# Performance work log

Measured on AMD Instinct MI355X. Metric: run time of the kernel, lower is better.

The kernel has to match this reference:

```python
import jax, jax.numpy as jnp
import numpy as np

NMS_THRESH = 0.7
N_PRE = 12000
N_POST = 2000
IMG_X, IMG_Y = 1333.0, 402.0
MIN_SIZE = 16.0
FEAT_X, FEAT_Y, N_ANCH = 83, 25, 9   # int(1333/16), int(402/16), 9 anchors/cell
A = FEAT_X * FEAT_Y * N_ANCH         # 18675 anchors
CHUNK = 600                          # N_PRE % CHUNK == 0 -> 20 scan steps


def _make_anchors():
    stride = 16.0
    scales = np.array([8.0, 16.0, 32.0])
    ratios = np.array([0.5, 1.0, 2.0])
    hs = (stride * scales[:, None] * np.sqrt(ratios)[None, :]).ravel()  # 9 heights
    ws = (stride * scales[:, None] / np.sqrt(ratios)[None, :]).ravel()  # 9 widths
    cx = (np.arange(FEAT_X, dtype=np.float64) + 0.5) * stride
    cy = (np.arange(FEAT_Y, dtype=np.float64) + 0.5) * stride
    cxg, cyg = np.meshgrid(cx, cy, indexing="ij")  # [83,25]
    cxg = cxg[:, :, None]
    cyg = cyg[:, :, None]
    boxes = np.stack([cxg - 0.5 * ws, cyg - 0.5 * hs,
                      cxg + 0.5 * ws, cyg + 0.5 * hs], axis=-1)  # [83,25,9,4]
    return boxes.reshape(-1, 4).astype(np.float32)


def setup_inputs() -> dict:
    key = jax.random.key(0)
    k1, k2 = jax.random.split(key)
    return {
        "anchor_boxes": jnp.asarray(_make_anchors()),                          # [A,4]
        "rpn_cls_score": jax.random.normal(k1, (1, A, 2), jnp.float32),        # [B,A,2]
        "rpn_bbox_pred": jax.random.normal(k2, (1, A, 4), jnp.float32) * 0.1,  # [B,A,4]
    }


def _decode(anchor_boxes, rpn_cls_score, rpn_bbox_pred):
    # anchor geometry (same conventions as original: y from col1/3, x from col0/2)
    h_a = anchor_boxes[:, 3] - anchor_boxes[:, 1]
    w_a = anchor_boxes[:, 2] - anchor_boxes[:, 0]
    cy_a = anchor_boxes[:, 1] + 0.5 * h_a
    cx_a = anchor_boxes[:, 0] + 0.5 * w_a
    dx = rpn_bbox_pred[..., 0]
    dy = rpn_bbox_pred[..., 1]
    dw = rpn_bbox_pred[..., 2]
    dh = rpn_bbox_pred[..., 3]
    cy = dy * h_a + cy_a
    cx = dx * w_a + cx_a
    h = jnp.exp(dh) * h_a
    w = jnp.exp(dw) * w_a
    # clip: x coords to image_size[0], y coords to image_size[1] (as in original)
    x1 = jnp.clip(cx - 0.5 * w, 0.0, IMG_X)
    x2 = jnp.clip(cx + 0.5 * w, 0.0, IMG_X)
    y1 = jnp.clip(cy - 0.5 * h, 0.0, IMG_Y)
    y2 = jnp.clip(cy + 0.5 * h, 0.0, IMG_Y)
    roi = jnp.stack([x1, y1, x2, y2], axis=-1)  # [B,A,4]
    valid = ((y2 - y1) >= MIN_SIZE) & ((x2 - x1) >= MIN_SIZE)  # [B,A]
    score = rpn_cls_score[..., 1]  # objectness = channel 1 of 2-class score
    return roi, score, valid


def _nms_per_image(roi, score, valid):
    # sort valid boxes by descending score, take top N_PRE
    score = jnp.where(valid, score, -jnp.inf)
    order = jnp.argsort(-score)[:N_PRE]
    boxes = roi[order]  # [N_PRE,4]
    x1, y1, x2, y2 = boxes[:, 0], boxes[:, 1], boxes[:, 2], boxes[:, 3]
    areas = (x2 - x1 + 1.0) * (y2 - y1 + 1.0)
    idx = jnp.arange(N_PRE)

    def chunk_step(mark, zs):
        def row(z):
            xx1 = jnp.maximum(x1[z], x1)
            yy1 = jnp.maximum(y1[z], y1)
            xx2 = jnp.minimum(x2[z], x2)
            yy2 = jnp.minimum(y2[z], y2)
            w = jnp.maximum(0.0, xx2 - xx1 + 1.0)
            h = jnp.maximum(0.0, yy2 - yy1 + 1.0)
            inter = w * h
            ovr = inter / (areas[z] + areas - inter)
            over = ovr >= NMS_THRESH
            # faithful to original: np.where on the slice [z+1:] yields indices
            # RELATIVE to the slice, which are then used as absolute row indices.
            # So box k is deleted iff exists z with IoU(box z, box z+1+k) >= thresh.
            src = idx + z + 1
            contrib = jnp.where(src < N_PRE, over[jnp.minimum(src, N_PRE - 1)], False)
            return contrib & (z < N_PRE - 1)  # loop runs z in range(N_PRE-1)
        contribs = jax.vmap(row)(zs)  # [CHUNK, N_PRE]
        return mark | contribs.any(axis=0), None

    mark0 = jnp.zeros((N_PRE,), bool)
    mark, _ = jax.lax.scan(chunk_step, mark0, idx.reshape(-1, CHUNK))
    keep = ~mark
    # compact kept boxes to the front (stable), truncate to N_POST
    ord2 = jnp.argsort((~keep).astype(jnp.int32), stable=True)[:N_POST]
    kept = keep[ord2]
    out = jnp.where(kept[:, None], boxes[ord2], 0.0)  # zero-pad deleted slots
    return out, kept


def reference(anchor_boxes, rpn_cls_score, rpn_bbox_pred):
    roi, score, valid = _decode(anchor_boxes, rpn_cls_score, rpn_bbox_pred)
    rois, kept = jax.vmap(_nms_per_image)(roi, score, valid)
    return rois, kept  # [B,N_POST,4], [B,N_POST]
```

## Files before the change

kernel.cpp:

```cpp
#include <hip/hip_runtime.h>
#include <math.h>

#define A_TOT   18675
#define N_PRE   12000
#define N_POST  2000
#define IMG_X   1333.0f
#define IMG_Y   402.0f
#define MIN_SZ  16.0f
#define NMS_T   0.7f
#define NBUCK   4096
#define NBLK1   19

__global__ __launch_bounds__(1024)
void decode_hist_kernel(const float* __restrict__ anch,
                        const float* __restrict__ cls,
                        const float* __restrict__ pred,
                        float4* __restrict__ roi,
                        unsigned long long* __restrict__ key,
                        unsigned* __restrict__ phist,
                        unsigned* __restrict__ gcnt) {
    __shared__ unsigned lh[NBUCK];
    const int t   = threadIdx.x;
    const int blk = blockIdx.x;
    const int g   = blk * 1024 + t;

#pragma unroll
    for (int e = 0; e < 4; ++e) lh[t + e * 1024] = 0u;
    if (g < NBUCK) gcnt[g] = 0u;
    __syncthreads();

    if (g < A_TOT) {
        float ax1 = anch[4*g+0], ay1 = anch[4*g+1], ax2 = anch[4*g+2], ay2 = anch[4*g+3];
        float h_a  = __fsub_rn(ay2, ay1);
        float w_a  = __fsub_rn(ax2, ax1);
        float cy_a = __fadd_rn(ay1, __fmul_rn(0.5f, h_a));
        float cx_a = __fadd_rn(ax1, __fmul_rn(0.5f, w_a));

        float dx = pred[4*g+0], dy = pred[4*g+1], dw = pred[4*g+2], dh = pred[4*g+3];

        float cy = __fadd_rn(__fmul_rn(dy, h_a), cy_a);
        float cx = __fadd_rn(__fmul_rn(dx, w_a), cx_a);
        float h  = __fmul_rn(expf(dh), h_a);
        float w  = __fmul_rn(expf(dw), w_a);

        float hw = __fmul_rn(0.5f, w);
        float hh = __fmul_rn(0.5f, h);
        float x1 = fminf(fmaxf(__fsub_rn(cx, hw), 0.0f), IMG_X);
        float x2 = fminf(fmaxf(__fadd_rn(cx, hw), 0.0f), IMG_X);
        float y1 = fminf(fmaxf(__fsub_rn(cy, hh), 0.0f), IMG_Y);
        float y2 = fminf(fmaxf(__fadd_rn(cy, hh), 0.0f), IMG_Y);

        bool valid = (__fsub_rn(y2, y1) >= MIN_SZ) && (__fsub_rn(x2, x1) >= MIN_SZ);

        roi[g] = make_float4(x1, y1, x2, y2);

        float s = valid ? cls[2*g+1] : -INFINITY;
        unsigned ub   = __float_as_uint(s);
        unsigned mask = ((unsigned)((int)ub >> 31)) | 0x80000000u;
        unsigned ord  = ub ^ mask;
        unsigned kd   = ~ord;
        key[g] = ((unsigned long long)kd << 32) | (unsigned)g;
        atomicAdd(&lh[kd >> 20], 1u);
    }
    __syncthreads();

    ((uint4*)phist)[blk * 1024 + t] =
        make_uint4(lh[4*t+0], lh[4*t+1], lh[4*t+2], lh[4*t+3]);
}

__global__ __launch_bounds__(1024)
void scan_scatter_kernel(const unsigned long long* __restrict__ key,
                         const unsigned* __restrict__ phist,
                         unsigned* __restrict__ gcnt,
                         unsigned* __restrict__ ghist,
                         unsigned* __restrict__ gbstart,
                         unsigned long long* __restrict__ bkey) {
    __shared__ unsigned bs[NBUCK];
    __shared__ unsigned wsum[16];
    const int t    = threadIdx.x;
    const int blk  = blockIdx.x;
    const int lane = t & 63;
    const int wv   = t >> 6;

    unsigned c0 = 0, c1 = 0, c2 = 0, c3 = 0;
#pragma unroll
    for (int k = 0; k < NBLK1; ++k) {
        uint4 v = ((const uint4*)phist)[k * 1024 + t];
        c0 += v.x; c1 += v.y; c2 += v.z; c3 += v.w;
    }
    unsigned mysum = c0 + c1 + c2 + c3;

    unsigned incl = mysum;
#pragma unroll
    for (int off = 1; off < 64; off <<= 1) {
        unsigned v = __shfl_up(incl, off, 64);
        if (lane >= off) incl += v;
    }
    if (lane == 63) wsum[wv] = incl;
    __syncthreads();
    if (t == 0) {
        unsigned run = 0;
        for (int k = 0; k < 16; ++k) { unsigned v = wsum[k]; wsum[k] = run; run += v; }
    }
    __syncthreads();

    unsigned base = wsum[wv] + (incl - mysum);
    unsigned s0 = base, s1 = s0 + c0, s2 = s1 + c1, s3 = s2 + c2;
    bs[4*t+0] = s0; bs[4*t+1] = s1; bs[4*t+2] = s2; bs[4*t+3] = s3;

    if (blk == 0) {
        ((uint4*)gbstart)[t] = make_uint4(s0, s1, s2, s3);
        ((uint4*)ghist)[t]   = make_uint4(c0, c1, c2, c3);
    }
    __syncthreads();

    int g = blk * 1024 + t;
    if (g < A_TOT) {
        unsigned long long Ki = key[g];
        unsigned b = (unsigned)(Ki >> 52);
        unsigned pos = bs[b] + atomicAdd(&gcnt[b], 1u);
        bkey[pos] = Ki;
    }
}

__global__ void rankscatter_kernel(const unsigned long long* __restrict__ bkey,
                                   const unsigned* __restrict__ gbstart,
                                   const unsigned* __restrict__ ghist,
                                   const float4* __restrict__ roi,
                                   float4* __restrict__ sboxes,
                                   float* __restrict__ sareas) {
    int g = blockIdx.x * blockDim.x + threadIdx.x;
    int p = g >> 6;
    int lane = g & 63;
    if (p >= A_TOT) return;

    unsigned long long Ki = bkey[p];
    unsigned b = (unsigned)(Ki >> 52);
    unsigned start = gbstart[b];
    if (start >= N_PRE) return;
    unsigned cnt = ghist[b];

    unsigned r = start;
    for (unsigned m = 0; m < cnt; m += 64) {
        unsigned mm = m + lane;
        bool lt = (mm < cnt) && (bkey[start + mm] < Ki);
        r += (unsigned)__popcll(__ballot(lt));
    }

    if (lane == 0 && r < N_PRE) {
        unsigned idx = (unsigned)Ki;
        float4 bx = roi[idx];
        sboxes[r] = bx;
        sareas[r] = __fmul_rn(__fadd_rn(__fsub_rn(bx.z, bx.x), 1.0f),
                              __fadd_rn(__fsub_rn(bx.w, bx.y), 1.0f));
    }
}

__global__ void nms_kernel(const float4* __restrict__ sboxes,
                           const float* __restrict__ sareas,
                           unsigned* __restrict__ mark) {
    int wid  = (blockIdx.x * blockDim.x + threadIdx.x) >> 6;
    int lane = threadIdx.x & 63;
    if (wid >= N_PRE) return;
    const int i      = wid;
    const int npairs = N_PRE - 1 - i;

    bool found = false;
    for (int base = 0; base < npairs; base += 64) {
        int z = base + lane;
        bool over = false;
        if (z < npairs) {
            float4 bz = sboxes[z];
            float4 bj = sboxes[z + i + 1];
            float az = sareas[z];
            float aj = sareas[z + i + 1];
            float xx1 = fmaxf(bz.x, bj.x);
            float yy1 = fmaxf(bz.y, bj.y);
            float xx2 = fminf(bz.z, bj.z);
            float yy2 = fminf(bz.w, bj.w);
            float w = fmaxf(0.0f, __fadd_rn(__fsub_rn(xx2, xx1), 1.0f));
            float h = fmaxf(0.0f, __fadd_rn(__fsub_rn(yy2, yy1), 1.0f));
            float inter = __fmul_rn(w, h);
            float denom = __fsub_rn(__fadd_rn(az, aj), inter);
            float ovr   = __fdiv_rn(inter, denom);
            over = (ovr >= NMS_T);
        }
        if (__any(over)) { found = true; break; }
    }
    if (lane == 0) mark[i] = found ? 1u : 0u;
}

__global__ __launch_bounds__(1024)
void output_kernel(const unsigned* __restrict__ mark,
                   const float4* __restrict__ sboxes,
                   float* __restrict__ out) {
    __shared__ int wsA[16];
    __shared__ int wsB[16];
    __shared__ int wsS[16];
    __shared__ int s_base, s_total;
    const int t    = threadIdx.x;
    const int blk  = blockIdx.x;
    const int lane = t & 63;
    const int wv   = t >> 6;
    const int limit = blk * 1024;

    int sum_before = 0, sum_total = 0;
    for (int j = t; j < N_PRE; j += 1024) {
        int k = (mark[j] == 0u) ? 1 : 0;
        sum_total += k;
        if (j < limit) sum_before += k;
    }
#pragma unroll
    for (int off = 32; off > 0; off >>= 1) {
        sum_before += __shfl_xor(sum_before, off, 64);
        sum_total  += __shfl_xor(sum_total,  off, 64);
    }
    if (lane == 0) { wsA[wv] = sum_before; wsB[wv] = sum_total; }
    __syncthreads();
    if (t == 0) {
        int a = 0, b = 0;
        for (int k = 0; k < 16; ++k) { a += wsA[k]; b += wsB[k]; }
        s_base = a; s_total = b;
    }
    __syncthreads();

    const int i = blk * 1024 + t;
    int keep = (i < N_PRE) && (mark[i] == 0u);

    int incl = keep;
#pragma unroll
    for (int off = 1; off < 64; off <<= 1) {
        int v = __shfl_up(incl, off, 64);
        if (lane >= off) incl += v;
    }
    if (lane == 63) wsS[wv] = incl;
    __syncthreads();
    if (t == 0) {
        int run = 0;
        for (int k = 0; k < 16; ++k) { int v = wsS[k]; wsS[k] = run; run += v; }
    }
    __syncthreads();

    int pos = s_base + wsS[wv] + (incl - keep);
    if (keep && pos < N_POST) {
        float4 b4 = sboxes[i];
        out[4*pos+0] = b4.x;
        out[4*pos+1] = b4.y;
        out[4*pos+2] = b4.z;
        out[4*pos+3] = b4.w;
        out[4*N_POST + pos] = 1.0f;
    }
    if (i < N_POST && i >= s_total) {
        out[4*i+0] = 0.0f; out[4*i+1] = 0.0f;
        out[4*i+2] = 0.0f; out[4*i+3] = 0.0f;
        out[4*N_POST + i] = 0.0f;
    }
}

extern "C" void kernel_launch(void* const* d_in, const int* in_sizes, int n_in,
                              void* d_out, int out_size, void* d_ws, size_t ws_size,
                              hipStream_t stream) {
    const float* anch = (const float*)d_in[0];
    const float* cls  = (const float*)d_in[1];
    const float* pred = (const float*)d_in[2];
    float* out = (float*)d_out;

    char* ws = (char*)d_ws;
    float4*             roi     = (float4*)(ws + 0);
    unsigned long long* key     = (unsigned long long*)(ws + 299008);
    unsigned*           phist   = (unsigned*)(ws + 448512);
    unsigned*           gcnt    = (unsigned*)(ws + 759808);
    unsigned*           ghist   = (unsigned*)(ws + 776192);
    unsigned*           gbstart = (unsigned*)(ws + 792576);
    unsigned long long* bkey    = (unsigned long long*)(ws + 808960);
    float4*             sboxes  = (float4*)(ws + 958464);
    float*              sareas  = (float*)(ws + 1150464);
    unsigned*           mark    = (unsigned*)(ws + 1198464);

    const int TB = 256;
    const int rblk = (A_TOT * 64 + TB - 1) / TB;

    decode_hist_kernel<<<NBLK1, 1024, 0, stream>>>(anch, cls, pred, roi, key, phist, gcnt);
    scan_scatter_kernel<<<NBLK1, 1024, 0, stream>>>(key, phist, gcnt, ghist, gbstart, bkey);
    rankscatter_kernel<<<rblk, TB, 0, stream>>>(bkey, gbstart, ghist, roi, sboxes, sareas);
    nms_kernel<<<(N_PRE * 64) / TB, TB, 0, stream>>>(sboxes, sareas, mark);
    output_kernel<<<12, 1024, 0, stream>>>(mark, sboxes, out);
}
```

Before: 57.96 us.

## Fuse all proposal stages into one cooperative kernel with grid-wide syncs

Replaces the five separate launches (decode/histogram, scan/scatter, rank-scatter, NMS, output compaction) with a single cooperative kernel of 256 blocks of 1024 threads that separates the stages with grid.sync(). The per-block partial histograms become one global histogram built with global atomics, and every block recomputes the bucket prefix scan in shared memory. The rank and NMS loops become grid-stride loops over waves. This removes four kernel launch gaps and the partial-histogram pass. In exchange it adds grid-wide barriers, contended global atomics and a cooperative launch whose 256x1024 residency must be supported.

After: 177.7 us. 207% more time.

```diff
diff --git a/kernel.cpp b/kernel.cpp
--- a/kernel.cpp
+++ b/kernel.cpp
@@ -1,4 +1,5 @@
 #include <hip/hip_runtime.h>
+#include <hip/hip_cooperative_groups.h>
 #include <math.h>
 
 #define A_TOT   18675
@@ -9,25 +10,43 @@
 #define MIN_SZ  16.0f
 #define NMS_T   0.7f
 #define NBUCK   4096
-#define NBLK1   19
-
-__global__ __launch_bounds__(1024)
-void decode_hist_kernel(const float* __restrict__ anch,
-                        const float* __restrict__ cls,
-                        const float* __restrict__ pred,
-                        float4* __restrict__ roi,
-                        unsigned long long* __restrict__ key,
-                        unsigned* __restrict__ phist,
-                        unsigned* __restrict__ gcnt) {
-    __shared__ unsigned lh[NBUCK];
-    const int t   = threadIdx.x;
-    const int blk = blockIdx.x;
-    const int g   = blk * 1024 + t;
-
-#pragma unroll
-    for (int e = 0; e < 4; ++e) lh[t + e * 1024] = 0u;
-    if (g < NBUCK) gcnt[g] = 0u;
-    __syncthreads();
+#define GBLK    256
+#define NTHR    1024
+#define NWAVES  (GBLK * (NTHR / 64))
+
+namespace cg = cooperative_groups;
+
+__global__ __launch_bounds__(NTHR)
+void fused_kernel(const float* __restrict__ anch,
+                  const float* __restrict__ cls,
+                  const float* __restrict__ pred,
+                  float4* __restrict__ roi,
+                  unsigned long long* __restrict__ key,
+                  unsigned* __restrict__ ghist,
+                  unsigned* __restrict__ gcnt,
+                  unsigned long long* __restrict__ bkey,
+                  float4* __restrict__ sboxes,
+                  float* __restrict__ sareas,
+                  unsigned* __restrict__ mark,
+                  float* __restrict__ out)
+{
+    cg::grid_group grid = cg::this_grid();
+
+    __shared__ unsigned bs[NBUCK];
+    __shared__ unsigned lcnt[NBUCK];
+    __shared__ unsigned wsum[16];
+    __shared__ int wsA[16], wsB[16], wsS[16];
+    __shared__ int s_base, s_total;
+
+    const int t    = threadIdx.x;
+    const int blk  = blockIdx.x;
+    const int g    = blk * NTHR + t;
+    const int lane = t & 63;
+    const int wv   = t >> 6;
+    const int gw   = blk * (NTHR / 64) + wv;
+
+    if (g < NBUCK) { ghist[g] = 0u; gcnt[g] = 0u; }
+    grid.sync();
 
     if (g < A_TOT) {
         float ax1 = anch[4*g+0], ay1 = anch[4*g+1], ax2 = anch[4*g+2], ay2 = anch[4*g+3];
@@ -60,200 +79,148 @@
         unsigned ord  = ub ^ mask;
         unsigned kd   = ~ord;
         key[g] = ((unsigned long long)kd << 32) | (unsigned)g;
-        atomicAdd(&lh[kd >> 20], 1u);
-    }
-    __syncthreads();
-
-    ((uint4*)phist)[blk * 1024 + t] =
-        make_uint4(lh[4*t+0], lh[4*t+1], lh[4*t+2], lh[4*t+3]);
-}
-
-__global__ __launch_bounds__(1024)
-void scan_scatter_kernel(const unsigned long long* __restrict__ key,
-                         const unsigned* __restrict__ phist,
-                         unsigned* __restrict__ gcnt,
-                         unsigned* __restrict__ ghist,
-                         unsigned* __restrict__ gbstart,
-                         unsigned long long* __restrict__ bkey) {
-    __shared__ unsigned bs[NBUCK];
-    __shared__ unsigned wsum[16];
-    const int t    = threadIdx.x;
-    const int blk  = blockIdx.x;
-    const int lane = t & 63;
-    const int wv   = t >> 6;
-
-    unsigned c0 = 0, c1 = 0, c2 = 0, c3 = 0;
+        atomicAdd(&ghist[kd >> 20], 1u);
+    }
+    grid.sync();
+
+    {
+        uint4 v = ((const uint4*)ghist)[t];
+        unsigned c0 = v.x, c1 = v.y, c2 = v.z, c3 = v.w;
+        unsigned mysum = c0 + c1 + c2 + c3;
+        unsigned incl = mysum;
 #pragma unroll
-    for (int k = 0; k < NBLK1; ++k) {
-        uint4 v = ((const uint4*)phist)[k * 1024 + t];
-        c0 += v.x; c1 += v.y; c2 += v.z; c3 += v.w;
-    }
-    unsigned mysum = c0 + c1 + c2 + c3;
-
-    unsigned incl = mysum;
-#pragma unroll
-    for (int off = 1; off < 64; off <<= 1) {
-        unsigned v = __shfl_up(incl, off, 64);
-        if (lane >= off) incl += v;
-    }
-    if (lane == 63) wsum[wv] = incl;
-    __syncthreads();
-    if (t == 0) {
-        unsigned run = 0;
-        for (int k = 0; k < 16; ++k) { unsigned v = wsum[k]; wsum[k] = run; run += v; }
-    }
-    __syncthreads();
-
-    unsigned base = wsum[wv] + (incl - mysum);
-    unsigned s0 = base, s1 = s0 + c0, s2 = s1 + c1, s3 = s2 + c2;
-    bs[4*t+0] = s0; bs[4*t+1] = s1; bs[4*t+2] = s2; bs[4*t+3] = s3;
-
-    if (blk == 0) {
-        ((uint4*)gbstart)[t] = make_uint4(s0, s1, s2, s3);
-        ((uint4*)ghist)[t]   = make_uint4(c0, c1, c2, c3);
-    }
-    __syncthreads();
-
-    int g = blk * 1024 + t;
+        for (int off = 1; off < 64; off <<= 1) {
+            unsigned x = __shfl_up(incl, off, 64);
+            if (lane >= off) incl += x;
+        }
+        if (lane == 63) wsum[wv] = incl;
+        __syncthreads();
+        if (t == 0) {
+            unsigned run = 0;
+            for (int k = 0; k < 16; ++k) { unsigned x = wsum[k]; wsum[k] = run; run += x; }
+        }
+        __syncthreads();
+        unsigned base = wsum[wv] + (incl - mysum);
+        bs[4*t+0] = base;
+        bs[4*t+1] = base + c0;
+        bs[4*t+2] = base + c0 + c1;
+        bs[4*t+3] = base + c0 + c1 + c2;
+        lcnt[4*t+0] = c0; lcnt[4*t+1] = c1; lcnt[4*t+2] = c2; lcnt[4*t+3] = c3;
+        __syncthreads();
+    }
+
     if (g < A_TOT) {
         unsigned long long Ki = key[g];
         unsigned b = (unsigned)(Ki >> 52);
         unsigned pos = bs[b] + atomicAdd(&gcnt[b], 1u);
         bkey[pos] = Ki;
     }
-}
-
-__global__ void rankscatter_kernel(const unsigned long long* __restrict__ bkey,
-                                   const unsigned* __restrict__ gbstart,
-                                   const unsigned* __restrict__ ghist,
-                                   const float4* __restrict__ roi,
-                                   float4* __restrict__ sboxes,
-                                   float* __restrict__ sareas) {
-    int g = blockIdx.x * blockDim.x + threadIdx.x;
-    int p = g >> 6;
-    int lane = g & 63;
-    if (p >= A_TOT) return;
-
-    unsigned long long Ki = bkey[p];
-    unsigned b = (unsigned)(Ki >> 52);
-    unsigned start = gbstart[b];
-    if (start >= N_PRE) return;
-    unsigned cnt = ghist[b];
-
-    unsigned r = start;
-    for (unsigned m = 0; m < cnt; m += 64) {
-        unsigned mm = m + lane;
-        bool lt = (mm < cnt) && (bkey[start + mm] < Ki);
-        r += (unsigned)__popcll(__ballot(lt));
-    }
-
-    if (lane == 0 && r < N_PRE) {
-        unsigned idx = (unsigned)Ki;
-        float4 bx = roi[idx];
-        sboxes[r] = bx;
-        sareas[r] = __fmul_rn(__fadd_rn(__fsub_rn(bx.z, bx.x), 1.0f),
-                              __fadd_rn(__fsub_rn(bx.w, bx.y), 1.0f));
-    }
-}
-
-__global__ void nms_kernel(const float4* __restrict__ sboxes,
-                           const float* __restrict__ sareas,
-                           unsigned* __restrict__ mark) {
-    int wid  = (blockIdx.x * blockDim.x + threadIdx.x) >> 6;
-    int lane = threadIdx.x & 63;
-    if (wid >= N_PRE) return;
-    const int i      = wid;
-    const int npairs = N_PRE - 1 - i;
-
-    bool found = false;
-    for (int base = 0; base < npairs; base += 64) {
-        int z = base + lane;
-        bool over = false;
-        if (z < npairs) {
-            float4 bz = sboxes[z];
-            float4 bj = sboxes[z + i + 1];
-            float az = sareas[z];
-            float aj = sareas[z + i + 1];
-            float xx1 = fmaxf(bz.x, bj.x);
-            float yy1 = fmaxf(bz.y, bj.y);
-            float xx2 = fminf(bz.z, bj.z);
-            float yy2 = fminf(bz.w, bj.w);
-            float w = fmaxf(0.0f, __fadd_rn(__fsub_rn(xx2, xx1), 1.0f));
-            float h = fmaxf(0.0f, __fadd_rn(__fsub_rn(yy2, yy1), 1.0f));
-            float inter = __fmul_rn(w, h);
-            float denom = __fsub_rn(__fadd_rn(az, aj), inter);
-            float ovr   = __fdiv_rn(inter, denom);
-            over = (ovr >= NMS_T);
-        }
-        if (__any(over)) { found = true; break; }
-    }
-    if (lane == 0) mark[i] = found ? 1u : 0u;
-}
-
-__global__ __launch_bounds__(1024)
-void output_kernel(const unsigned* __restrict__ mark,
-                   const float4* __restrict__ sboxes,
-                   float* __restrict__ out) {
-    __shared__ int wsA[16];
-    __shared__ int wsB[16];
-    __shared__ int wsS[16];
-    __shared__ int s_base, s_total;
-    const int t    = threadIdx.x;
-    const int blk  = blockIdx.x;
-    const int lane = t & 63;
-    const int wv   = t >> 6;
-    const int limit = blk * 1024;
-
-    int sum_before = 0, sum_total = 0;
-    for (int j = t; j < N_PRE; j += 1024) {
-        int k = (mark[j] == 0u) ? 1 : 0;
-        sum_total += k;
-        if (j < limit) sum_before += k;
-    }
+    grid.sync();
+
+    for (int p = gw; p < A_TOT; p += NWAVES) {
+        unsigned long long Ki = bkey[p];
+        unsigned b = (unsigned)(Ki >> 52);
+        unsigned start = bs[b];
+        if (start >= N_PRE) continue;
+        unsigned cnt = lcnt[b];
+        unsigned r = start;
+        for (unsigned m = 0; m < cnt; m += 64) {
+            unsigned mm = m + lane;
+            bool lt = (mm < cnt) && (bkey[start + mm] < Ki);
+            r += (unsigned)__popcll(__ballot(lt));
+        }
+        if (lane == 0 && r < N_PRE) {
+            unsigned idx = (unsigned)Ki;
+            float4 bx = roi[idx];
+            sboxes[r] = bx;
+            sareas[r] = __fmul_rn(__fadd_rn(__fsub_rn(bx.z, bx.x), 1.0f),
+                                  __fadd_rn(__fsub_rn(bx.w, bx.y), 1.0f));
+        }
+    }
+    grid.sync();
+
+    for (int i = gw; i < N_PRE; i += NWAVES) {
+        const int npairs = N_PRE - 1 - i;
+        bool found = false;
+        for (int base0 = 0; base0 < npairs; base0 += 64) {
+            int z = base0 + lane;
+            bool over = false;
+            if (z < npairs) {
+                float4 bz = sboxes[z];
+                float4 bj = sboxes[z + i + 1];
+                float az = sareas[z];
+                float aj = sareas[z + i + 1];
+                float xx1 = fmaxf(bz.x, bj.x);
+                float yy1 = fmaxf(bz.y, bj.y);
+                float xx2 = fminf(bz.z, bj.z);
+                float yy2 = fminf(bz.w, bj.w);
+                float w = fmaxf(0.0f, __fadd_rn(__fsub_rn(xx2, xx1), 1.0f));
+                float h = fmaxf(0.0f, __fadd_rn(__fsub_rn(yy2, yy1), 1.0f));
+                float inter = __fmul_rn(w, h);
+                float denom = __fsub_rn(__fadd_rn(az, aj), inter);
+                float ovr   = __fdiv_rn(inter, denom);
+                over = (ovr >= NMS_T);
+            }
+            if (__any(over)) { found = true; break; }
+        }
+        if (lane == 0) mark[i] = found ? 1u : 0u;
+    }
+    grid.sync();
+
+    if (blk < 12) {
+        const int limit = blk * NTHR;
+
+        int sum_before = 0, sum_total = 0;
+        for (int j = t; j < N_PRE; j += NTHR) {
+            int k = (mark[j] == 0u) ? 1 : 0;
+            sum_total += k;
+            if (j < limit) sum_before += k;
+        }
 #pragma unroll
-    for (int off = 32; off > 0; off >>= 1) {
-        sum_before += __shfl_xor(sum_before, off, 64);
-        sum_total  += __shfl_xor(sum_total,  off, 64);
-    }
-    if (lane == 0) { wsA[wv] = sum_before; wsB[wv] = sum_total; }
-    __syncthreads();
-    if (t == 0) {
-        int a = 0, b = 0;
-        for (int k = 0; k < 16; ++k) { a += wsA[k]; b += wsB[k]; }
-        s_base = a; s_total = b;
-    }
-    __syncthreads();
-
-    const int i = blk * 1024 + t;
-    int keep = (i < N_PRE) && (mark[i] == 0u);
-
-    int incl = keep;
+        for (int off = 32; off > 0; off >>= 1) {
+            sum_before += __shfl_xor(sum_before, off, 64);
+            sum_total  += __shfl_xor(sum_total,  off, 64);
+        }
+        if (lane == 0) { wsA[wv] = sum_before; wsB[wv] = sum_total; }
+        __syncthreads();
+        if (t == 0) {
+            int a = 0, b = 0;
+            for (int k = 0; k < 16; ++k) { a += wsA[k]; b += wsB[k]; }
+            s_base = a; s_total = b;
+        }
+        __syncthreads();
+
+        const int i = blk * NTHR + t;
+        int keep = (i < N_PRE) && (mark[i] == 0u);
+
+        int incl = keep;
 #pragma unroll
-    for (int off = 1; off < 64; off <<= 1) {
-        int v = __shfl_up(incl, off, 64);
-        if (lane >= off) incl += v;
-    }
-    if (lane == 63) wsS[wv] = incl;
-    __syncthreads();
-    if (t == 0) {
-        int run = 0;
-        for (int k = 0; k < 16; ++k) { int v = wsS[k]; wsS[k] = run; run += v; }
-    }
-    __syncthreads();
-
-    int pos = s_base + wsS[wv] + (incl - keep);
-    if (keep && pos < N_POST) {
-        float4 b4 = sboxes[i];
-        out[4*pos+0] = b4.x;
-        out[4*pos+1] = b4.y;
-        out[4*pos+2] = b4.z;
-        out[4*pos+3] = b4.w;
-        out[4*N_POST + pos] = 1.0f;
-    }
-    if (i < N_POST && i >= s_total) {
-        out[4*i+0] = 0.0f; out[4*i+1] = 0.0f;
-        out[4*i+2] = 0.0f; out[4*i+3] = 0.0f;
-        out[4*N_POST + i] = 0.0f;
+        for (int off = 1; off < 64; off <<= 1) {
+            int x = __shfl_up(incl, off, 64);
+            if (lane >= off) incl += x;
+        }
+        if (lane == 63) wsS[wv] = incl;
+        __syncthreads();
+        if (t == 0) {
+            int run = 0;
+            for (int k = 0; k < 16; ++k) { int x = wsS[k]; wsS[k] = run; run += x; }
+        }
+        __syncthreads();
+
+        int pos = s_base + wsS[wv] + (incl - keep);
+        if (keep && pos < N_POST) {
+            float4 b4 = sboxes[i];
+            out[4*pos+0] = b4.x;
+            out[4*pos+1] = b4.y;
+            out[4*pos+2] = b4.z;
+            out[4*pos+3] = b4.w;
+            out[4*N_POST + pos] = 1.0f;
+        }
+        if (i < N_POST && i >= s_total) {
+            out[4*i+0] = 0.0f; out[4*i+1] = 0.0f;
+            out[4*i+2] = 0.0f; out[4*i+3] = 0.0f;
+            out[4*N_POST + i] = 0.0f;
+        }
     }
 }
 
@@ -266,23 +233,20 @@
     float* out = (float*)d_out;
 
     char* ws = (char*)d_ws;
-    float4*             roi     = (float4*)(ws + 0);
-    unsigned long long* key     = (unsigned long long*)(ws + 299008);
-    unsigned*           phist   = (unsigned*)(ws + 448512);
-    unsigned*           gcnt    = (unsigned*)(ws + 759808);
-    unsigned*           ghist   = (unsigned*)(ws + 776192);
-    unsigned*           gbstart = (unsigned*)(ws + 792576);
-    unsigned long long* bkey    = (unsigned long long*)(ws + 808960);
-    float4*             sboxes  = (float4*)(ws + 958464);
-    float*              sareas  = (float*)(ws + 1150464);
-    unsigned*           mark    = (unsigned*)(ws + 1198464);
-
-    const int TB = 256;
-    const int rblk = (A_TOT * 64 + TB - 1) / TB;
-
-    decode_hist_kernel<<<NBLK1, 1024, 0, stream>>>(anch, cls, pred, roi, key, phist, gcnt);
-    scan_scatter_kernel<<<NBLK1, 1024, 0, stream>>>(key, phist, gcnt, ghist, gbstart, bkey);
-    rankscatter_kernel<<<rblk, TB, 0, stream>>>(bkey, gbstart, ghist, roi, sboxes, sareas);
-    nms_kernel<<<(N_PRE * 64) / TB, TB, 0, stream>>>(sboxes, sareas, mark);
-    output_kernel<<<12, 1024, 0, stream>>>(mark, sboxes, out);
+    float4*             roi    = (float4*)(ws + 0);
+    unsigned long long* key    = (unsigned long long*)(ws + 299008);
+    unsigned*           ghist  = (unsigned*)(ws + 448512);
+    unsigned*           gcnt   = (unsigned*)(ws + 464896);
+    unsigned long long* bkey   = (unsigned long long*)(ws + 481280);
+    float4*             sboxes = (float4*)(ws + 630784);
+    float*              sareas = (float*)(ws + 822784);
+    unsigned*           mark   = (unsigned*)(ws + 870784);
+
+    void* args[] = {
+        (void*)&anch, (void*)&cls, (void*)&pred,
+        (void*)&roi, (void*)&key, (void*)&ghist, (void*)&gcnt,
+        (void*)&bkey, (void*)&sboxes, (void*)&sareas, (void*)&mark, (void*)&out
+    };
+    hipLaunchCooperativeKernel((const void*)fused_kernel,
+                               dim3(GBLK), dim3(NTHR), args, 0, stream);
 }
```
